# Kernel optimization log

Hardware: AMD Instinct MI355X
Metric: run time of the kernel (lower is better)

## Reference

```python
import jax, jax.numpy as jnp
import numpy as np

N = 8192      # total nodes = B * NPG
D = 512       # in_dim = hidden_dim = out_dim
E = 131072    # edges
B = 16        # graphs (selected_idx batch)
NPG = 512     # nodes per graph
S = 128       # selected nodes per graph
L = 3         # conv layers
EPS = 1e-5


def setup_inputs() -> dict:
    key = jax.random.key(0)
    ks = jax.random.split(key, 16)
    scale = 0.02
    return {
        "x": jax.random.normal(ks[0], (N, D), dtype=jnp.float32),
        "edge_index": jax.random.randint(ks[1], (2, E), 0, N),
        "selected_idx": jax.random.randint(ks[2], (B, S), 0, NPG),
        "edge_label": jax.random.randint(ks[3], (E,), 0, 4),
        # per-layer EdgeConv MLP params (stacked over L layers)
        "conv_W1": jax.random.normal(ks[4], (L, 2 * D, D), dtype=jnp.float32) * scale,
        "conv_b1": jnp.full((L, D), 0.01, dtype=jnp.float32),
        "conv_W2": jax.random.normal(ks[5], (L, D, D), dtype=jnp.float32) * scale,
        "conv_b2": jnp.full((L, D), 0.01, dtype=jnp.float32),
        # shared layer norms
        "ln1_g": jnp.ones((D,), dtype=jnp.float32),
        "ln1_b": jnp.zeros((D,), dtype=jnp.float32),
        "ln2_g": jnp.ones((D,), dtype=jnp.float32),
        "ln2_b": jnp.zeros((D,), dtype=jnp.float32),
        # final FFN
        "ffn_W1": jax.random.normal(ks[6], (D, D), dtype=jnp.float32) * scale,
        "ffn_b1": jnp.full((D,), 0.01, dtype=jnp.float32),
        "ffn_W2": jax.random.normal(ks[7], (D, D), dtype=jnp.float32) * scale,
        "ffn_b2": jnp.full((D,), 0.01, dtype=jnp.float32),
    }


def _layer_norm(x, g, b):
    mu = jnp.mean(x, axis=-1, keepdims=True)
    var = jnp.mean(jnp.square(x - mu), axis=-1, keepdims=True)
    return (x - mu) * jax.lax.rsqrt(var + EPS) * g + b


def reference(x, edge_index, selected_idx, edge_label,
              conv_W1, conv_b1, conv_W2, conv_b2,
              ln1_g, ln1_b, ln2_g, ln2_b,
              ffn_W1, ffn_b1, ffn_W2, ffn_b2):
    src = edge_index[0]  # x_j source nodes
    dst = edge_index[1]  # x_i target nodes (aggregation index)
    for l in range(L):
        residual = x
        h = _layer_norm(x, ln1_g, ln1_b)
        hi = h[dst]                                   # [E, D]
        hj = h[src]                                   # [E, D]
        ef = jnp.concatenate([hi, hj - hi], axis=1)   # [E, 2D]
        m = jnp.maximum(ef @ conv_W1[l] + conv_b1[l], 0.0) @ conv_W2[l] + conv_b2[l]
        agg = jax.ops.segment_max(m, dst, num_segments=N)  # max-aggregate [N, D]
        agg = jnp.where(jnp.isfinite(agg), agg, 0.0)       # nodes w/o in-edges -> 0
        x = jnp.maximum(agg, 0.0) + residual
    residual = x
    h = _layer_norm(x, ln2_g, ln2_b)
    y = jnp.maximum(h @ ffn_W1 + ffn_b1, 0.0) @ ffn_W2 + ffn_b2
    x = y + residual
    x = x.reshape(B, NPG, D)
    idx = jnp.broadcast_to(selected_idx[:, :, None], (B, S, D))
    return jnp.take_along_axis(x, idx, axis=1)  # [B, S, D]
```

## Files before the change

### kernel.cpp

```cpp
#include <hip/hip_runtime.h>
#include <stdint.h>

#define NN 8192
#define DD 512
#define EE 131072
#define BBATCH 16
#define NPG 512
#define SSEL 128
#define LL 3

typedef unsigned short u16;
typedef __bf16 bf16x8 __attribute__((ext_vector_type(8)));
typedef float f32x4 __attribute__((ext_vector_type(4)));
typedef float f32x2 __attribute__((ext_vector_type(2)));
typedef u16 u16x8 __attribute__((ext_vector_type(8)));

__device__ __forceinline__ float bf2f(u16 u) {
    union { unsigned i; float f; } v; v.i = ((unsigned)u) << 16; return v.f;
}
__device__ __forceinline__ u16 f2bf(float f) {
    union { unsigned i; float f; } v; v.f = f;
    unsigned i = v.i;
    return (u16)((i + 0x7FFFu + ((i >> 16) & 1u)) >> 16);
}

__device__ __forceinline__ unsigned pk_bf16(float s0, float s1) {
#if __has_builtin(__builtin_amdgcn_cvt_pk_bf16_f32)
    typedef __bf16 bf16x2 __attribute__((ext_vector_type(2)));
    union { bf16x2 v; unsigned u; } r;
    r.v = __builtin_amdgcn_cvt_pk_bf16_f32(s0, s1);
    return r.u;
#else
    unsigned r0 = __float_as_uint(s0);
    r0 = (r0 + 0x7FFFu + ((r0 >> 16) & 1u)) >> 16;
    unsigned r1 = __float_as_uint(s1);
    r1 = (r1 + 0x7FFFu + ((r1 >> 16) & 1u)) & 0xffff0000u;
    return r0 | r1;
#endif
}

__device__ __forceinline__ void async_cp16(const u16* g, u16* l) {
    __builtin_amdgcn_global_load_lds(
        (const __attribute__((address_space(1))) unsigned int*)g,
        (__attribute__((address_space(3))) unsigned int*)l, 16, 0, 0);
}

__global__ __launch_bounds__(256) void ln_fused(const float* __restrict__ xin,
                                                float* __restrict__ agg_io,
                                                float* __restrict__ xout,
                                                const float* __restrict__ g,
                                                const float* __restrict__ b,
                                                u16* __restrict__ h, int doAdd) {
    int row = blockIdx.x * 4 + (threadIdx.x >> 6);
    int lane = threadIdx.x & 63;
    const f32x4* x4 = (const f32x4*)(xin + (size_t)row * DD);
    f32x4 p = x4[lane * 2], q = x4[lane * 2 + 1];
    if (doAdd) {
        const f32x4* a4 = (const f32x4*)(agg_io + (size_t)row * DD);
        f32x4 pa = a4[lane * 2], qa = a4[lane * 2 + 1];
        #pragma unroll
        for (int i = 0; i < 4; ++i) { p[i] += pa[i]; q[i] += qa[i]; }
    }
    if (agg_io) {
        f32x4 z;
        #pragma unroll
        for (int i = 0; i < 4; ++i) z[i] = 0.f;
        f32x4* a4 = (f32x4*)(agg_io + (size_t)row * DD);
        a4[lane * 2] = z;
        a4[lane * 2 + 1] = z;
    }
    f32x4* xo = (f32x4*)(xout + (size_t)row * DD);
    xo[lane * 2] = p;
    xo[lane * 2 + 1] = q;
    float v[8];
    v[0] = p[0]; v[1] = p[1]; v[2] = p[2]; v[3] = p[3];
    v[4] = q[0]; v[5] = q[1]; v[6] = q[2]; v[7] = q[3];
    float s = 0.f, sq = 0.f;
    #pragma unroll
    for (int i = 0; i < 8; ++i) { s += v[i]; sq += v[i] * v[i]; }
    #pragma unroll
    for (int o = 32; o >= 1; o >>= 1) { s += __shfl_xor(s, o); sq += __shfl_xor(sq, o); }
    float mu = s * (1.f / DD);
    float var = sq * (1.f / DD) - mu * mu;
    float rs = rsqrtf(var + 1e-5f);
    int kb = lane * 8;
    u16x8 o8;
    #pragma unroll
    for (int i = 0; i < 8; ++i) o8[i] = f2bf((v[i] - mu) * rs * g[kb + i] + b[kb + i]);
    *(u16x8*)(h + (size_t)row * DD + kb) = o8;
}

__global__ void hist_kernel(const int* __restrict__ dst, int* __restrict__ cnt) {
    int e = blockIdx.x * 256 + threadIdx.x;
    if (e < EE) atomicAdd(&cnt[dst[e]], 1);
}

__global__ __launch_bounds__(1024) void scan_kernel(const int* __restrict__ cnt,
                                                    int* __restrict__ off,
                                                    int* __restrict__ cur) {
    __shared__ int part[1024];
    int t = threadIdx.x;
    int base = t * 8;
    int loc[8]; int s = 0;
    #pragma unroll
    for (int i = 0; i < 8; ++i) { loc[i] = s; s += cnt[base + i]; }
    part[t] = s;
    __syncthreads();
    for (int o = 1; o < 1024; o <<= 1) {
        int v = part[t];
        int u = (t >= o) ? part[t - o] : 0;
        __syncthreads();
        part[t] = v + u;
        __syncthreads();
    }
    int bx = (t > 0) ? part[t - 1] : 0;
    #pragma unroll
    for (int i = 0; i < 8; ++i) { off[base + i] = bx + loc[i]; cur[base + i] = bx + loc[i]; }
    if (t == 0) off[NN] = part[1023];
}

__global__ void scatter_kernel(const int* __restrict__ src, const int* __restrict__ dst,
                               int* __restrict__ cur, int* __restrict__ ssrc,
                               int* __restrict__ sdst) {
    int e = blockIdx.x * 256 + threadIdx.x;
    if (e < EE) {
        int d = dst[e];
        int p = atomicAdd(&cur[d], 1);
        ssrc[p] = src[e];
        sdst[p] = d;
    }
}

struct CvtJobs {
    const float* s[5];
    u16* d[5];
};
__global__ __launch_bounds__(256) void cvt_t5_kernel(CvtJobs jobs) {
    __shared__ u16 tile[32][33];
    const float* src = jobs.s[blockIdx.z];
    u16* dstp = jobs.d[blockIdx.z];
    int bk = blockIdx.x * 32, bn = blockIdx.y * 32;
    int tx = threadIdx.x & 31, ty = threadIdx.x >> 5;
    #pragma unroll
    for (int r = 0; r < 32; r += 8)
        tile[ty + r][tx] = f2bf(src[(size_t)(bk + ty + r) * 512 + bn + tx]);
    __syncthreads();
    #pragma unroll
    for (int r = 0; r < 32; r += 8)
        dstp[(size_t)(bn + ty + r) * 512 + bk + tx] = tile[tx][ty + r];
}

__global__ __launch_bounds__(256) void cvt_w1_kernel(const float* __restrict__ W1g,
                                                     u16* __restrict__ dstg) {
    __shared__ u16 tile[32][33];
    const float* W1 = W1g + (size_t)blockIdx.z * 1024 * 512;
    u16* dstp = dstg + (size_t)blockIdx.z * 1024 * 512;
    int bk = blockIdx.x * 32, bn = blockIdx.y * 32;
    int tx = threadIdx.x & 31, ty = threadIdx.x >> 5;
    #pragma unroll
    for (int r = 0; r < 32; r += 8) {
        int k = bk + ty + r, n = bn + tx;
        float v = (n < 512) ? (W1[(size_t)k * 512 + n] - W1[(size_t)(k + 512) * 512 + n])
                            : W1[(size_t)(k + 512) * 512 + (n - 512)];
        tile[ty + r][tx] = f2bf(v);
    }
    __syncthreads();
    #pragma unroll
    for (int r = 0; r < 32; r += 8)
        dstp[(size_t)(bn + ty + r) * 512 + bk + tx] = tile[tx][ty + r];
}

template <int EMODE>
__global__ __launch_bounds__(256) void gemm_async(
    const u16* __restrict__ A, const u16* __restrict__ BT,
    const float* __restrict__ bias, const float* __restrict__ resid,
    void* __restrict__ Cout, int K, int ldc) {
    __shared__ u16 lA[128 * 64];
    __shared__ u16 lB[128 * 64];
    const int tid = threadIdx.x;
    const int lane = tid & 63, wave = tid >> 6;
    const int wm = wave & 1, wn = wave >> 1;
    const int quad = lane >> 4, lm = lane & 15;
    const int tileM = blockIdx.x, tileN = blockIdx.y;

    const int g = (lane & 7) ^ (lane >> 3);
    const u16* ap[4];
    const u16* bp[4];
    u16* lad[4];
    u16* lbd[4];
    #pragma unroll
    for (int j = 0; j < 4; ++j) {
        int seg = wave * 4 + j;
        int rA = tileM * 128 + seg * 8 + (lane >> 3);
        int rB = tileN * 128 + seg * 8 + (lane >> 3);
        ap[j] = A + (size_t)rA * K + g * 8;
        bp[j] = BT + (size_t)rB * K + g * 8;
        lad[j] = lA + seg * 512;
        lbd[j] = lB + seg * 512;
    }

    f32x4 acc[4][4];
    #pragma unroll
    for (int mt = 0; mt < 4; ++mt)
        #pragma unroll
        for (int nt = 0; nt < 4; ++nt)
            #pragma unroll
            for (int j = 0; j < 4; ++j) acc[mt][nt][j] = 0.f;

    for (int kb = 0; kb < K; kb += 64) {
        #pragma unroll
        for (int j = 0; j < 4; ++j) {
            async_cp16(ap[j], lad[j]);
            async_cp16(bp[j], lbd[j]);
            ap[j] += 64;
            bp[j] += 64;
        }
        __syncthreads();
        #pragma unroll
        for (int kk = 0; kk < 64; kk += 32) {
            bf16x8 af[4], bfr[4];
            int gbase = (kk >> 3) + quad;
            #pragma unroll
            for (int mt = 0; mt < 4; ++mt) {
                int row = wm * 64 + mt * 16 + lm;
                af[mt] = *(const bf16x8*)(lA + row * 64 + ((gbase ^ (row & 7)) << 3));
            }
            #pragma unroll
            for (int nt = 0; nt < 4; ++nt) {
                int row = wn * 64 + nt * 16 + lm;
                bfr[nt] = *(const bf16x8*)(lB + row * 64 + ((gbase ^ (row & 7)) << 3));
            }
            #pragma unroll
            for (int mt = 0; mt < 4; ++mt)
                #pragma unroll
                for (int nt = 0; nt < 4; ++nt)
                    acc[mt][nt] = __builtin_amdgcn_mfma_f32_16x16x32_bf16(
                        af[mt], bfr[nt], acc[mt][nt], 0, 0, 0);
        }
        __syncthreads();
    }
    #pragma unroll
    for (int mt = 0; mt < 4; ++mt) {
        #pragma unroll
        for (int nt = 0; nt < 4; ++nt) {
            int col = tileN * 128 + wn * 64 + nt * 16 + lm;
            float bv;
            if (EMODE == 2) bv = 0.f;
            else if (EMODE == 3) bv = (col < 512) ? bias[col] : 0.f;
            else bv = bias[col];
            #pragma unroll
            for (int j = 0; j < 4; ++j) {
                int grow = tileM * 128 + wm * 64 + mt * 16 + quad * 4 + j;
                float v = acc[mt][nt][j] + bv;
                if (EMODE == 0) {
                    ((u16*)Cout)[(size_t)grow * ldc + col] = f2bf(fmaxf(v, 0.f));
                } else if (EMODE == 1) {
                    ((float*)Cout)[(size_t)grow * ldc + col] =
                        v + resid[(size_t)grow * ldc + col];
                } else {
                    ((u16*)Cout)[(size_t)grow * ldc + col] = f2bf(v);
                }
            }
        }
    }
}

__global__ __launch_bounds__(512, 4) void gemm_edge(
    const u16* __restrict__ P, const int* __restrict__ ssrc,
    const int* __restrict__ sdst, const u16* __restrict__ W2T,
    const float* __restrict__ b2, float* __restrict__ agg) {
    __shared__ u16 smem[64 * 64 + 512 * 64];
    __shared__ int nid_l[64];
    u16* lA = smem;
    u16* lB = smem + 64 * 64;
    const int tid = threadIdx.x;
    const int lane = tid & 63, wave = tid >> 6;
    const int quad = lane >> 4, lm = lane & 15;
    const int ebase = blockIdx.x * 64;

    if (tid < 64) nid_l[tid] = sdst[ebase + tid];

    const int g = (lane & 7) ^ (lane >> 3);
    int aoff, boff, lout;
    {
        int row = wave * 8 + (lane >> 3);
        int dn = sdst[ebase + row];
        int sn = ssrc[ebase + row];
        aoff = dn * 1024 + g * 8;
        boff = sn * 1024 + 512 + g * 8;
        lout = wave * 512 + lane * 8;
    }
    int wbase, lbbase;
    {
        int row0 = wave * 64 + (lane >> 3);
        wbase = row0 * 512 + g * 8;
        lbbase = wave * 4096;
    }

    f32x4 acc[4][4];
    #pragma unroll
    for (int mt = 0; mt < 4; ++mt)
        #pragma unroll
        for (int nt = 0; nt < 4; ++nt)
            #pragma unroll
            for (int j = 0; j < 4; ++j) acc[mt][nt][j] = 0.f;

    for (int kb = 0; kb < 512; kb += 64) {
        u16x8 ga = *(const u16x8*)(P + aoff + kb);
        u16x8 gb = *(const u16x8*)(P + boff + kb);
        #pragma unroll
        for (int j = 0; j < 8; ++j)
            async_cp16(W2T + wbase + j * 4096 + kb, lB + lbbase + j * 512);
        {
            union { u16x8 v; unsigned w[4]; } ua, ub;
            ua.v = ga;
            ub.v = gb;
            unsigned o[4];
            #pragma unroll
            for (int q = 0; q < 4; ++q) {
                f32x2 a, c;
                a[0] = __uint_as_float(ua.w[q] << 16);
                a[1] = __uint_as_float(ua.w[q] & 0xffff0000u);
                c[0] = __uint_as_float(ub.w[q] << 16);
                c[1] = __uint_as_float(ub.w[q] & 0xffff0000u);
                f32x2 s = a + c;
#if __has_builtin(__builtin_elementwise_max)
                f32x2 z; z[0] = 0.f; z[1] = 0.f;
                s = __builtin_elementwise_max(s, z);
#else
                s[0] = fmaxf(s[0], 0.f);
                s[1] = fmaxf(s[1], 0.f);
#endif
                o[q] = pk_bf16(s[0], s[1]);
            }
            *(uint4*)(lA + lout) = make_uint4(o[0], o[1], o[2], o[3]);
        }
        __syncthreads();
        #pragma unroll
        for (int kk = 0; kk < 64; kk += 32) {
            bf16x8 af[4], bfr[4];
            int gbase = (kk >> 3) + quad;
            #pragma unroll
            for (int mt = 0; mt < 4; ++mt) {
                int row = mt * 16 + lm;
                af[mt] = *(const bf16x8*)(lA + row * 64 + ((gbase ^ (row & 7)) << 3));
            }
            #pragma unroll
            for (int nt = 0; nt < 4; ++nt) {
                int row = wave * 64 + nt * 16 + lm;
                bfr[nt] = *(const bf16x8*)(lB + row * 64 + ((gbase ^ (row & 7)) << 3));
            }
            #pragma unroll
            for (int mt = 0; mt < 4; ++mt)
                #pragma unroll
                for (int nt = 0; nt < 4; ++nt)
                    acc[mt][nt] = __builtin_amdgcn_mfma_f32_16x16x32_bf16(
                        af[mt], bfr[nt], acc[mt][nt], 0, 0, 0);
        }
        __syncthreads();
    }

    u16* cbuf = smem;
    #pragma unroll
    for (int nt = 0; nt < 4; ++nt) {
        int col = wave * 64 + nt * 16 + lm;
        float bv = b2[col];
        #pragma unroll
        for (int mt = 0; mt < 4; ++mt) {
            #pragma unroll
            for (int j2 = 0; j2 < 4; ++j2) {
                int row = mt * 16 + quad * 4 + j2;
                cbuf[row * 520 + col] = f2bf(fmaxf(acc[mt][nt][j2] + bv, 0.f));
            }
        }
    }
    __syncthreads();
    {
        int col = tid;
        int cur = nid_l[0];
        float run = bf2f(cbuf[col]);
        for (int r = 1; r < 64; ++r) {
            int nd = nid_l[r];
            float v = bf2f(cbuf[r * 520 + col]);
            if (nd != cur) {
                atomicMax((unsigned int*)&agg[(size_t)cur * DD + col],
                          __float_as_uint(run));
                cur = nd;
                run = v;
            } else {
                run = fmaxf(run, v);
            }
        }
        atomicMax((unsigned int*)&agg[(size_t)cur * DD + col],
                  __float_as_uint(run));
    }
}

__global__ __launch_bounds__(128) void gather_fused(const float* __restrict__ x,
                                                    const float* __restrict__ agg,
                                                    const int* __restrict__ sel,
                                                    float* __restrict__ xs) {
    int i = blockIdx.x;
    int b = i >> 7;
    int r = b * NPG + sel[i];
    const f32x4* srcp = (const f32x4*)(x + (size_t)r * DD);
    const f32x4* aggp = (const f32x4*)(agg + (size_t)r * DD);
    f32x4 v = srcp[threadIdx.x];
    f32x4 a = aggp[threadIdx.x];
    #pragma unroll
    for (int j = 0; j < 4; ++j) v[j] += a[j];
    ((f32x4*)(xs + (size_t)i * DD))[threadIdx.x] = v;
}

extern "C" void kernel_launch(void* const* d_in, const int* in_sizes, int n_in,
                              void* d_out, int out_size, void* d_ws, size_t ws_size,
                              hipStream_t stream) {
    const float* x_in = (const float*)d_in[0];
    const int* ei = (const int*)d_in[1];
    const int* sel = (const int*)d_in[2];
    const float* W1 = (const float*)d_in[4];
    const float* b1 = (const float*)d_in[5];
    const float* W2 = (const float*)d_in[6];
    const float* b2 = (const float*)d_in[7];
    const float* g1 = (const float*)d_in[8];
    const float* be1 = (const float*)d_in[9];
    const float* g2 = (const float*)d_in[10];
    const float* be2 = (const float*)d_in[11];
    const float* fW1 = (const float*)d_in[12];
    const float* fb1 = (const float*)d_in[13];
    const float* fW2 = (const float*)d_in[14];
    const float* fb2 = (const float*)d_in[15];
    float* out = (float*)d_out;

    char* w = (char*)d_ws;
    size_t off = 0;
    auto alloc = [&](size_t bytes) -> char* {
        char* p = w + off;
        off += (bytes + 255) & ~(size_t)255;
        return p;
    };
    float* xbuf = (float*)alloc((size_t)NN * DD * 4);
    float* agg  = (float*)alloc((size_t)NN * DD * 4);
    u16* h      = (u16*)alloc((size_t)NN * DD * 2);
    u16* P      = (u16*)alloc((size_t)NN * 1024 * 2);
    u16* W1T    = (u16*)alloc((size_t)LL * 1024 * DD * 2);
    u16* W2T    = (u16*)alloc((size_t)LL * DD * DD * 2);
    u16* FW1T   = (u16*)alloc((size_t)DD * DD * 2);
    u16* FW2T   = (u16*)alloc((size_t)DD * DD * 2);
    int* cnt    = (int*)alloc((size_t)NN * 4);
    int* offs   = (int*)alloc((size_t)(NN + 1) * 4);
    int* cur    = (int*)alloc((size_t)NN * 4);
    int* ssrc   = (int*)alloc((size_t)EE * 4);
    int* sdst   = (int*)alloc((size_t)EE * 4);
    float* xs   = (float*)alloc((size_t)BBATCH * SSEL * DD * 4);
    u16* hs     = (u16*)alloc((size_t)BBATCH * SSEL * DD * 2);
    u16* uu     = (u16*)alloc((size_t)BBATCH * SSEL * DD * 2);

    const int* esrc = ei;
    const int* edst = ei + EE;

    hipMemsetAsync(cnt, 0, (size_t)NN * 4, stream);
    hist_kernel<<<EE / 256, 256, 0, stream>>>(edst, cnt);
    scan_kernel<<<1, 1024, 0, stream>>>(cnt, offs, cur);
    scatter_kernel<<<EE / 256, 256, 0, stream>>>(esrc, edst, cur, ssrc, sdst);

    cvt_w1_kernel<<<dim3(16, 32, LL), 256, 0, stream>>>(W1, W1T);
    {
        CvtJobs jobs;
        jobs.s[0] = W2;
        jobs.s[1] = W2 + (size_t)DD * DD;
        jobs.s[2] = W2 + (size_t)2 * DD * DD;
        jobs.s[3] = fW1;
        jobs.s[4] = fW2;
        jobs.d[0] = W2T;
        jobs.d[1] = W2T + (size_t)DD * DD;
        jobs.d[2] = W2T + (size_t)2 * DD * DD;
        jobs.d[3] = FW1T;
        jobs.d[4] = FW2T;
        cvt_t5_kernel<<<dim3(16, 16, 5), 256, 0, stream>>>(jobs);
    }

    for (int l = 0; l < LL; ++l) {
        ln_fused<<<NN / 4, 256, 0, stream>>>(l == 0 ? x_in : xbuf, agg, xbuf, g1, be1,
                                             h, l > 0 ? 1 : 0);
        {
            dim3 grid(NN / 128, 1024 / 128);
            gemm_async<3><<<grid, 256, 0, stream>>>(
                h, W1T + (size_t)l * 1024 * DD, b1 + (size_t)l * DD, nullptr, P, DD,
                1024);
        }
        gemm_edge<<<EE / 64, 512, 0, stream>>>(
            P, ssrc, sdst, W2T + (size_t)l * DD * DD, b2 + (size_t)l * DD, agg);
    }

    gather_fused<<<BBATCH * SSEL, 128, 0, stream>>>(xbuf, agg, sel, xs);
    ln_fused<<<BBATCH * SSEL / 4, 256, 0, stream>>>(xs, nullptr, xs, g2, be2, hs, 0);
    dim3 gridf(BBATCH * SSEL / 128, DD / 128);
    gemm_async<0><<<gridf, 256, 0, stream>>>(hs, FW1T, fb1, nullptr, uu, DD, DD);
    gemm_async<1><<<gridf, 256, 0, stream>>>(uu, FW2T, fb2, xs, out, DD, DD);
}
```

Baseline: 551.0 us.

## Double-buffer edge GEMM K-loop with async W2 prefetch and smaller K tiles

Restructures the edge GEMM main loop to use K=32 tiles in two LDS buffers. The next W2T tile is prefetched asynchronously and the next gathered A tile is built while the MFMAs run on the current buffer, leaving one barrier per iteration instead of two. This aims to hide global-load latency behind compute, at the cost of twice as many loop iterations and smaller per-thread loads (uint2 instead of 16-byte vectors) for the gathered node rows.

Result: slower. 599.4 us (+8.8%).

```diff
diff --git a/kernel.cpp b/kernel.cpp
--- a/kernel.cpp
+++ b/kernel.cpp
@@ -45,6 +45,25 @@
         (__attribute__((address_space(3))) unsigned int*)l, 16, 0, 0);
 }
 
+__device__ __forceinline__ uint2 combine4(uint2 a, uint2 b) {
+    uint2 r;
+    unsigned wa[2] = {a.x, a.y}, wb[2] = {b.x, b.y};
+    unsigned ro[2];
+    #pragma unroll
+    for (int q = 0; q < 2; ++q) {
+        f32x2 s;
+        s[0] = __uint_as_float(wa[q] << 16) + __uint_as_float(wb[q] << 16);
+        s[1] = __uint_as_float(wa[q] & 0xffff0000u) +
+               __uint_as_float(wb[q] & 0xffff0000u);
+        s[0] = fmaxf(s[0], 0.f);
+        s[1] = fmaxf(s[1], 0.f);
+        ro[q] = pk_bf16(s[0], s[1]);
+    }
+    r.x = ro[0];
+    r.y = ro[1];
+    return r;
+}
+
 __global__ __launch_bounds__(256) void ln_fused(const float* __restrict__ xin,
                                                 float* __restrict__ agg_io,
                                                 float* __restrict__ xout,
@@ -269,10 +288,10 @@
     const u16* __restrict__ P, const int* __restrict__ ssrc,
     const int* __restrict__ sdst, const u16* __restrict__ W2T,
     const float* __restrict__ b2, float* __restrict__ agg) {
-    __shared__ u16 smem[64 * 64 + 512 * 64];
+    __shared__ u16 smem[2 * 64 * 32 + 2 * 512 * 32];
     __shared__ int nid_l[64];
     u16* lA = smem;
-    u16* lB = smem + 64 * 64;
+    u16* lB = smem + 2 * 64 * 32;
     const int tid = threadIdx.x;
     const int lane = tid & 63, wave = tid >> 6;
     const int quad = lane >> 4, lm = lane & 15;
@@ -280,84 +299,69 @@
 
     if (tid < 64) nid_l[tid] = sdst[ebase + tid];
 
-    const int g = (lane & 7) ^ (lane >> 3);
-    int aoff, boff, lout;
+    const int crow = tid >> 3, sub = tid & 7;
+    const int dn = sdst[ebase + crow];
+    const int sn = ssrc[ebase + crow];
+    const int aoff = dn * 1024 + sub * 4;
+    const int boff = sn * 1024 + 512 + sub * 4;
+    const int cwo = crow * 32 + (((sub >> 1) ^ (crow & 3)) << 3) + (sub & 1) * 4;
+
+    const int srow0 = wave * 64 + (lane >> 2);
+    const int gsrc = (lane & 3) ^ ((lane >> 2) & 3);
+    const int wbase = srow0 * 512 + gsrc * 8;
+    const int lbo = wave * 2048;
+
+    f32x4 acc[4][4];
+    #pragma unroll
+    for (int mt = 0; mt < 4; ++mt)
+        #pragma unroll
+        for (int nt = 0; nt < 4; ++nt)
+            #pragma unroll
+            for (int j = 0; j < 4; ++j) acc[mt][nt][j] = 0.f;
+
     {
-        int row = wave * 8 + (lane >> 3);
-        int dn = sdst[ebase + row];
-        int sn = ssrc[ebase + row];
-        aoff = dn * 1024 + g * 8;
-        boff = sn * 1024 + 512 + g * 8;
-        lout = wave * 512 + lane * 8;
-    }
-    int wbase, lbbase;
-    {
-        int row0 = wave * 64 + (lane >> 3);
-        wbase = row0 * 512 + g * 8;
-        lbbase = wave * 4096;
-    }
-
-    f32x4 acc[4][4];
-    #pragma unroll
-    for (int mt = 0; mt < 4; ++mt)
+        uint2 ua = *(const uint2*)(P + aoff);
+        uint2 ub = *(const uint2*)(P + boff);
+        *(uint2*)(lA + cwo) = combine4(ua, ub);
+    }
+    #pragma unroll
+    for (int j = 0; j < 4; ++j)
+        async_cp16(W2T + wbase + j * 8192, lB + lbo + j * 512);
+    asm volatile("s_waitcnt vmcnt(0) lgkmcnt(0)" ::: "memory");
+    __builtin_amdgcn_s_barrier();
+
+    for (int kb = 0; kb < 16; ++kb) {
+        const int cur = kb & 1, nxt = cur ^ 1;
+        const u16* lAc = lA + cur * 2048;
+        const u16* lBc = lB + cur * 16384;
+        if (kb < 15) {
+            #pragma unroll
+            for (int j = 0; j < 4; ++j)
+                async_cp16(W2T + wbase + j * 8192 + (kb + 1) * 32,
+                           lB + nxt * 16384 + lbo + j * 512);
+        }
+        __builtin_amdgcn_sched_barrier(0);
+        bf16x8 af[4], bfr[4];
+        const int gso = (quad ^ (lm & 3)) << 3;
+        #pragma unroll
+        for (int mt = 0; mt < 4; ++mt)
+            af[mt] = *(const bf16x8*)(lAc + (mt * 16 + lm) * 32 + gso);
         #pragma unroll
         for (int nt = 0; nt < 4; ++nt)
-            #pragma unroll
-            for (int j = 0; j < 4; ++j) acc[mt][nt][j] = 0.f;
-
-    for (int kb = 0; kb < 512; kb += 64) {
-        u16x8 ga = *(const u16x8*)(P + aoff + kb);
-        u16x8 gb = *(const u16x8*)(P + boff + kb);
-        #pragma unroll
-        for (int j = 0; j < 8; ++j)
-            async_cp16(W2T + wbase + j * 4096 + kb, lB + lbbase + j * 512);
-        {
-            union { u16x8 v; unsigned w[4]; } ua, ub;
-            ua.v = ga;
-            ub.v = gb;
-            unsigned o[4];
-            #pragma unroll
-            for (int q = 0; q < 4; ++q) {
-                f32x2 a, c;
-                a[0] = __uint_as_float(ua.w[q] << 16);
-                a[1] = __uint_as_float(ua.w[q] & 0xffff0000u);
-                c[0] = __uint_as_float(ub.w[q] << 16);
-                c[1] = __uint_as_float(ub.w[q] & 0xffff0000u);
-                f32x2 s = a + c;
-#if __has_builtin(__builtin_elementwise_max)
-                f32x2 z; z[0] = 0.f; z[1] = 0.f;
-                s = __builtin_elementwise_max(s, z);
-#else
-                s[0] = fmaxf(s[0], 0.f);
-                s[1] = fmaxf(s[1], 0.f);
-#endif
-                o[q] = pk_bf16(s[0], s[1]);
-            }
-            *(uint4*)(lA + lout) = make_uint4(o[0], o[1], o[2], o[3]);
-        }
-        __syncthreads();
-        #pragma unroll
-        for (int kk = 0; kk < 64; kk += 32) {
-            bf16x8 af[4], bfr[4];
-            int gbase = (kk >> 3) + quad;
-            #pragma unroll
-            for (int mt = 0; mt < 4; ++mt) {
-                int row = mt * 16 + lm;
-                af[mt] = *(const bf16x8*)(lA + row * 64 + ((gbase ^ (row & 7)) << 3));
-            }
-            #pragma unroll
-            for (int nt = 0; nt < 4; ++nt) {
-                int row = wave * 64 + nt * 16 + lm;
-                bfr[nt] = *(const bf16x8*)(lB + row * 64 + ((gbase ^ (row & 7)) << 3));
-            }
-            #pragma unroll
-            for (int mt = 0; mt < 4; ++mt)
-                #pragma unroll
-                for (int nt = 0; nt < 4; ++nt)
-                    acc[mt][nt] = __builtin_amdgcn_mfma_f32_16x16x32_bf16(
-                        af[mt], bfr[nt], acc[mt][nt], 0, 0, 0);
-        }
-        __syncthreads();
+            bfr[nt] = *(const bf16x8*)(lBc + (wave * 64 + nt * 16 + lm) * 32 + gso);
+        #pragma unroll
+        for (int mt = 0; mt < 4; ++mt)
+            #pragma unroll
+            for (int nt = 0; nt < 4; ++nt)
+                acc[mt][nt] = __builtin_amdgcn_mfma_f32_16x16x32_bf16(
+                    af[mt], bfr[nt], acc[mt][nt], 0, 0, 0);
+        if (kb < 15) {
+            uint2 ua = *(const uint2*)(P + aoff + (kb + 1) * 32);
+            uint2 ub = *(const uint2*)(P + boff + (kb + 1) * 32);
+            *(uint2*)(lA + nxt * 2048 + cwo) = combine4(ua, ub);
+        }
+        asm volatile("s_waitcnt vmcnt(0) lgkmcnt(0)" ::: "memory");
+        __builtin_amdgcn_s_barrier();
     }
 
     u16* cbuf = smem;
```
